# Kernel tuning notes

Hardware: AMD Instinct MI355X
Metric: run time of the kernel (lower is better)

Reference implementation:

```python
import jax, jax.numpy as jnp
import numpy as np

N_NODES = 100000
N_REL = 8
F_IN, F_HID, F_OUT = 64, 64, 32
N_EDGES = 1000000


def rgcn_conv(x, W, root, bias, src, dst, edge_type):
    """PyG RGCNConv with default aggr='mean': out[i] = sum_r mean_{j in N_r(i)} W_r x_j + root x_i + bias."""
    R, _, O = W.shape
    N = x.shape[0]
    # Transform every node under every relation: [R, N, O]
    h = jnp.einsum('nf,rfo->rno', x, W)
    # Gather per-edge messages: [E, O]
    msg = h[edge_type, src]
    # Per-(relation, dst) mean aggregation via combined segment ids
    seg = edge_type * N + dst
    sums = jax.ops.segment_sum(msg, seg, num_segments=R * N).reshape(R, N, O)
    cnt = jax.ops.segment_sum(jnp.ones((msg.shape[0],), msg.dtype), seg,
                              num_segments=R * N).reshape(R, N, 1)
    mean = sums / jnp.maximum(cnt, 1.0)  # empty neighborhoods -> 0
    return mean.sum(axis=0) + x @ root + bias


def setup_inputs() -> dict:
    key = jax.random.key(0)
    ks = jax.random.split(key, 9)
    s = lambda fan: 1.0 / np.sqrt(fan)
    x = jax.random.normal(ks[0], (N_NODES, F_IN), jnp.float32)
    edge_index = jax.random.randint(ks[1], (2, N_EDGES), 0, N_NODES, jnp.int64)
    edge_type = jax.random.randint(ks[2], (N_EDGES,), 0, N_REL, jnp.int64)
    W1 = jax.random.normal(ks[3], (N_REL, F_IN, F_HID), jnp.float32) * s(F_IN)
    root1 = jax.random.normal(ks[4], (F_IN, F_HID), jnp.float32) * s(F_IN)
    b1 = jnp.zeros((F_HID,), jnp.float32)
    W2 = jax.random.normal(ks[5], (N_REL, F_HID, F_OUT), jnp.float32) * s(F_HID)
    root2 = jax.random.normal(ks[6], (F_HID, F_OUT), jnp.float32) * s(F_HID)
    b2 = jnp.zeros((F_OUT,), jnp.float32)
    return {"x": x, "W1": W1, "root1": root1, "b1": b1,
            "W2": W2, "root2": root2, "b2": b2,
            "edge_index": edge_index, "edge_type": edge_type}


def reference(x, W1, root1, b1, W2, root2, b2, edge_index, edge_type):
    src, dst = edge_index[0], edge_index[1]
    # encode (dropout is identity in eval mode)
    h = jax.nn.relu(rgcn_conv(x, W1, root1, b1, src, dst, edge_type))
    z = rgcn_conv(h, W2, root2, b2, src, dst, edge_type)
    # decode: gather-dot-product link scores over the same edge list
    return (z[src] * z[dst]).sum(axis=1)
```

## Files before the change

kernel.cpp:

```cpp
#include <hip/hip_runtime.h>

#define F_IN 64
#define F_HID 64
#define F_OUT 32
#define NREL 8
#define SCAP 6144
#define RCAP 7680
#define MAXBUCK 200
#define PA_PE 16

typedef __attribute__((ext_vector_type(8))) short bfrag;
typedef __attribute__((ext_vector_type(4))) float ffrag;

__device__ inline unsigned short f2bf(float f) {
  unsigned u = __float_as_uint(f);
  unsigned r = (u + 0x7fffu + ((u >> 16) & 1u)) >> 16;
  return (unsigned short)r;
}
__device__ inline unsigned bf16pair(float lo, float hi) {
  return (unsigned)f2bf(lo) | ((unsigned)f2bf(hi) << 16);
}
__device__ inline float bflo(unsigned u) { return __uint_as_float(u << 16); }
__device__ inline float bfhi(unsigned u) { return __uint_as_float(u & 0xffff0000u); }

__device__ inline void acc8(float (&acc)[8], float s, uint4 g) {
  acc[0] += s * bflo(g.x); acc[1] += s * bfhi(g.x);
  acc[2] += s * bflo(g.y); acc[3] += s * bfhi(g.y);
  acc[4] += s * bflo(g.z); acc[5] += s * bfhi(g.z);
  acc[6] += s * bflo(g.w); acc[7] += s * bfhi(g.w);
}
__device__ inline float dot8(uint4 a, uint4 b) {
  return bflo(a.x) * bflo(b.x) + bfhi(a.x) * bfhi(b.x) +
         bflo(a.y) * bflo(b.y) + bfhi(a.y) * bfhi(b.y) +
         bflo(a.z) * bflo(b.z) + bfhi(a.z) * bfhi(b.z) +
         bflo(a.w) * bflo(b.w) + bfhi(a.w) * bfhi(b.w);
}

__global__ __launch_bounds__(256) void init_gcur(int* __restrict__ gcur, int nbuck) {
  int i = blockIdx.x * blockDim.x + threadIdx.x;
  if (i < nbuck) gcur[i] = i * SCAP;
}

__global__ __launch_bounds__(256) void binA_kernel(
    const int* __restrict__ src, const int* __restrict__ dst,
    const int* __restrict__ et, int* __restrict__ gcur,
    unsigned* __restrict__ staging, int E) {
  __shared__ int hist[MAXBUCK * 4];
  __shared__ int wbase[MAXBUCK * 4];
  const int tid = threadIdx.x;
  const int wave = tid >> 6;
  for (int i = tid; i < MAXBUCK * 4; i += 256) hist[i] = 0;
  __syncthreads();
  const int base = blockIdx.x * (256 * PA_PE);
  int dv[PA_PE], rk[PA_PE];
#pragma unroll
  for (int j = 0; j < PA_PE; ++j) {
    int e = base + j * 256 + tid;
    if (e < E) {
      int d = dst[e];
      dv[j] = d;
      rk[j] = atomicAdd(&hist[(d >> 9) * 4 + wave], 1);
    } else {
      dv[j] = -1;
    }
  }
  __syncthreads();
  for (int b = tid; b < MAXBUCK; b += 256) {
    int h0 = hist[b * 4 + 0], h1 = hist[b * 4 + 1];
    int h2 = hist[b * 4 + 2], h3 = hist[b * 4 + 3];
    int tot = h0 + h1 + h2 + h3;
    int gb = tot ? atomicAdd(&gcur[b], tot) : 0;
    wbase[b * 4 + 0] = gb;
    wbase[b * 4 + 1] = gb + h0;
    wbase[b * 4 + 2] = gb + h0 + h1;
    wbase[b * 4 + 3] = gb + h0 + h1 + h2;
  }
  __syncthreads();
#pragma unroll
  for (int j = 0; j < PA_PE; ++j) {
    if (dv[j] >= 0) {
      int e = base + j * 256 + tid;
      unsigned pk = (unsigned)src[e] | ((unsigned)et[e] << 17) |
                    ((unsigned)(dv[j] & 511) << 20);
      staging[wbase[(dv[j] >> 9) * 4 + wave] + rk[j]] = pk;
    }
  }
}

__global__ __launch_bounds__(256) void binB_kernel(
    const unsigned* __restrict__ staging, const int* __restrict__ gcur,
    int2* __restrict__ rec, int* __restrict__ startsA, int* __restrict__ endsA,
    int N) {
  __shared__ int cnt8[512 * 8];
  __shared__ int cur[512];
  __shared__ int tsum[256];
  const int b = blockIdx.x;
  const int tid = threadIdx.x;
  const int n0 = b << 9;
  const int nn = min(512, N - n0);
  const int cnt_b = gcur[b] - b * SCAP;
  const unsigned* st = staging + (size_t)b * SCAP;
  for (int i = tid; i < 512 * 8; i += 256) cnt8[i] = 0;
  __syncthreads();
  for (int i = tid; i < cnt_b; i += 256) {
    unsigned e = st[i];
    atomicAdd(&cnt8[((e >> 20) & 511) * 8 + ((e >> 17) & 7)], 1);
  }
  __syncthreads();
  const int na = 2 * tid, nb = 2 * tid + 1;
  int deg0 = 0, deg1 = 0;
#pragma unroll
  for (int r = 0; r < 8; ++r) {
    deg0 += cnt8[na * 8 + r];
    deg1 += cnt8[nb * 8 + r];
  }
  const int pd0 = (deg0 + 3) & ~3, pd1 = (deg1 + 3) & ~3;
  tsum[tid] = pd0 + pd1;
  __syncthreads();
  for (int off = 1; off < 256; off <<= 1) {
    int v = (tid >= off) ? tsum[tid - off] : 0;
    __syncthreads();
    tsum[tid] += v;
    __syncthreads();
  }
  const int excl = tsum[tid] - (pd0 + pd1);
  const int s0 = b * RCAP + excl;
  const int s1 = s0 + pd0;
  if (na < nn) { startsA[n0 + na] = s0; endsA[n0 + na] = s0 + pd0; cur[na] = s0; }
  if (nb < nn) { startsA[n0 + nb] = s1; endsA[n0 + nb] = s1 + pd1; cur[nb] = s1; }
  __syncthreads();
  for (int i = tid; i < 512 * 8; i += 256) {
    int cc = cnt8[i];
    ((float*)cnt8)[i] = cc > 0 ? 1.0f / (float)cc : 0.0f;
  }
  __syncthreads();
  for (int i = tid; i < cnt_b; i += 256) {
    unsigned e = st[i];
    int s = e & 0x1FFFF;
    int r = (e >> 17) & 7;
    int dl = (e >> 20) & 511;
    int pos = atomicAdd(&cur[dl], 1);
    rec[pos] = make_int2(r * N + s, ((const int*)cnt8)[dl * 8 + r]);
  }
  __syncthreads();
  if (na < nn) for (int p = cur[na]; p < s0 + pd0; ++p) rec[p] = make_int2(0, 0);
  if (nb < nn) for (int p = cur[nb]; p < s1 + pd1; ++p) rec[p] = make_int2(0, 0);
}

__global__ __launch_bounds__(256) void cvt_bf16_kernel(
    const float* __restrict__ in, unsigned* __restrict__ out, int n8) {
  int i = blockIdx.x * blockDim.x + threadIdx.x;
  if (i >= n8) return;
  const float4* p = (const float4*)(in + (size_t)i * 8);
  float4 a = p[0], b = p[1];
  uint4 o;
  o.x = bf16pair(a.x, a.y);
  o.y = bf16pair(a.z, a.w);
  o.z = bf16pair(b.x, b.y);
  o.w = bf16pair(b.z, b.w);
  *((uint4*)out + i) = o;
}

template <int O>
__global__ __launch_bounds__(256) void wprep_kernel(
    const float* __restrict__ W, unsigned short* __restrict__ Wf, int nrel) {
  constexpr int CT = O / 16;
  int t = blockIdx.x * blockDim.x + threadIdx.x;
  if (t >= nrel * CT * 2 * 64) return;
  int l = t & 63;
  int s = (t >> 6) & 1;
  int rc = t >> 7;
  int c = rc % CT;
  int r = rc / CT;
  const float* wsrc = W + (size_t)r * 64 * O;
  unsigned short* dst = Wf + (size_t)t * 8;
  int col = c * 16 + (l & 15);
  int k0 = s * 32 + ((l >> 4) * 8);
#pragma unroll
  for (int j = 0; j < 8; ++j) dst[j] = f2bf(wsrc[(size_t)(k0 + j) * O + col]);
}

template <int O>
__global__ __launch_bounds__(256) void mfma_transform_kernel(
    const unsigned short* __restrict__ Xb, const unsigned short* __restrict__ Wf,
    unsigned short* __restrict__ H, int N) {
  constexpr int CT = O / 16;
  constexpr int PAD = (O == 32) ? 40 : 72;
  __shared__ unsigned short tile[64 * PAD];
  const int w = threadIdx.x >> 6;
  const int l = threadIdx.x & 63;
  const int nb = blockIdx.x * 64;
  int arow = nb + w * 16 + (l & 15);
  if (arow >= N) arow = N - 1;
  const unsigned short* xp = Xb + (size_t)arow * 64 + ((l >> 4) * 8);
  bfrag a0 = *(const bfrag*)(xp);
  bfrag a1 = *(const bfrag*)(xp + 32);
  const int row = threadIdx.x >> 2, seg = threadIdx.x & 3;
  for (int r = 0; r < NREL + 1; ++r) {
    const unsigned short* wb = Wf + ((size_t)r * CT * 2 * 64 + l) * 8;
    ffrag acc[CT];
#pragma unroll
    for (int c = 0; c < CT; ++c) {
      bfrag b0 = *(const bfrag*)(wb + (size_t)(c * 2 + 0) * 512);
      bfrag b1 = *(const bfrag*)(wb + (size_t)(c * 2 + 1) * 512);
      ffrag z = {0.f, 0.f, 0.f, 0.f};
      acc[c] = __builtin_amdgcn_mfma_f32_16x16x32_bf16(a0, b0, z, 0, 0, 0);
      acc[c] = __builtin_amdgcn_mfma_f32_16x16x32_bf16(a1, b1, acc[c], 0, 0, 0);
    }
#pragma unroll
    for (int c = 0; c < CT; ++c)
#pragma unroll
      for (int i = 0; i < 4; ++i)
        tile[(w * 16 + (l >> 4) * 4 + i) * PAD + c * 16 + (l & 15)] = f2bf(acc[c][i]);
    __syncthreads();
    if (nb + row < N) {
      if (O == 64) {
        const uint4* sp = (const uint4*)(tile + row * PAD + seg * 16);
        uint4* gp = (uint4*)(H + ((size_t)r * N + nb + row) * 64 + seg * 16);
        gp[0] = sp[0];
        gp[1] = sp[1];
      } else {
        *(uint4*)(H + ((size_t)r * N + nb + row) * O + seg * 8) =
            *(const uint4*)(tile + row * PAD + seg * 8);
      }
    }
    __syncthreads();
  }
}

template <int O, bool RELU>
__global__ __launch_bounds__(256) void csr_agg_kernel(
    const unsigned* __restrict__ H, const int* __restrict__ startsA,
    const int* __restrict__ endsA, const int2* __restrict__ rec,
    const float* __restrict__ bias, unsigned* __restrict__ Y, int N) {
  constexpr int C = O / 8;
  constexpr int NPB = 256 / C;
  constexpr int HROW = O / 2;
  int t = threadIdx.x;
  int n = blockIdx.x * NPB + t / C;
  int c = t % C;
  if (n >= N) return;
  float acc[8];
  uint4 rr = *(const uint4*)(H + ((size_t)(NREL * N) + n) * HROW + c * 4);
  acc[0] = bias[c * 8 + 0] + bflo(rr.x);
  acc[1] = bias[c * 8 + 1] + bfhi(rr.x);
  acc[2] = bias[c * 8 + 2] + bflo(rr.y);
  acc[3] = bias[c * 8 + 3] + bfhi(rr.y);
  acc[4] = bias[c * 8 + 4] + bflo(rr.z);
  acc[5] = bias[c * 8 + 5] + bfhi(rr.z);
  acc[6] = bias[c * 8 + 6] + bflo(rr.w);
  acc[7] = bias[c * 8 + 7] + bfhi(rr.w);
  int p = startsA[n];
  int end = endsA[n];
  for (; p < end; p += 4) {
    int4 e01 = *(const int4*)(rec + p);
    int4 e23 = *(const int4*)(rec + p + 2);
    uint4 g0 = *(const uint4*)(H + (size_t)e01.x * HROW + c * 4);
    uint4 g1 = *(const uint4*)(H + (size_t)e01.z * HROW + c * 4);
    uint4 g2 = *(const uint4*)(H + (size_t)e23.x * HROW + c * 4);
    uint4 g3 = *(const uint4*)(H + (size_t)e23.z * HROW + c * 4);
    acc8(acc, __int_as_float(e01.y), g0);
    acc8(acc, __int_as_float(e01.w), g1);
    acc8(acc, __int_as_float(e23.y), g2);
    acc8(acc, __int_as_float(e23.w), g3);
  }
  if (RELU) {
#pragma unroll
    for (int j = 0; j < 8; ++j) acc[j] = fmaxf(acc[j], 0.f);
  }
  uint4 o;
  o.x = bf16pair(acc[0], acc[1]);
  o.y = bf16pair(acc[2], acc[3]);
  o.z = bf16pair(acc[4], acc[5]);
  o.w = bf16pair(acc[6], acc[7]);
  *(uint4*)(Y + (size_t)n * HROW + c * 4) = o;
}

__global__ __launch_bounds__(256) void decode_kernel(
    const unsigned* __restrict__ Z, const int* __restrict__ src,
    const int* __restrict__ dst, float* __restrict__ out, int E) {
  int e = blockIdx.x * blockDim.x + threadIdx.x;
  if (e >= E) return;
  const uint4* zs = (const uint4*)(Z + (size_t)src[e] * 16);
  const uint4* zd = (const uint4*)(Z + (size_t)dst[e] * 16);
  uint4 a0 = zs[0], a1 = zs[1], a2 = zs[2], a3 = zs[3];
  uint4 b0 = zd[0], b1 = zd[1], b2 = zd[2], b3 = zd[3];
  out[e] = dot8(a0, b0) + dot8(a1, b1) + dot8(a2, b2) + dot8(a3, b3);
}

extern "C" void kernel_launch(void* const* d_in, const int* in_sizes, int n_in,
                              void* d_out, int out_size, void* d_ws, size_t ws_size,
                              hipStream_t stream) {
  const float* x     = (const float*)d_in[0];
  const float* W1    = (const float*)d_in[1];
  const float* root1 = (const float*)d_in[2];
  const float* b1    = (const float*)d_in[3];
  const float* W2    = (const float*)d_in[4];
  const float* root2 = (const float*)d_in[5];
  const float* b2    = (const float*)d_in[6];
  const int*   ei    = (const int*)d_in[7];
  const int*   et    = (const int*)d_in[8];

  const int N = in_sizes[0] / F_IN;
  const int E = in_sizes[8];
  const int nbuck = (N + 511) >> 9;
  const int* srcp = ei;
  const int* dstp = ei + E;

  char* ws = (char*)d_ws;
  int*            gcur    = (int*)(ws + 0);
  unsigned*       staging = (unsigned*)(ws + 4096);
  int*            startsA = (int*)(ws + 4849664);
  int*            endsA   = (int*)(ws + 5249664);
  int2*           rec     = (int2*)(ws + 5649664);
  unsigned short* xb      = (unsigned short*)(ws + 17691904);
  unsigned short* wf1     = (unsigned short*)(ws + 30491904);
  unsigned short* wf2     = (unsigned short*)(ws + 30565632);
  unsigned short* h       = (unsigned short*)(ws + 30602496);
  unsigned short* hmid    = (unsigned short*)(ws + 145802496);
  unsigned short* z       = (unsigned short*)(ws + 158602496);

  init_gcur<<<1, 256, 0, stream>>>(gcur, nbuck);
  binA_kernel<<<(E + 256 * PA_PE - 1) / (256 * PA_PE), 256, 0, stream>>>(
      srcp, dstp, et, gcur, staging, E);
  binB_kernel<<<nbuck, 256, 0, stream>>>(staging, gcur, rec, startsA, endsA, N);

  cvt_bf16_kernel<<<(N * (F_IN / 8) + 255) / 256, 256, 0, stream>>>(
      x, (unsigned*)xb, N * (F_IN / 8));
  wprep_kernel<F_HID><<<16, 256, 0, stream>>>(W1, wf1, NREL);
  wprep_kernel<F_HID><<<2, 256, 0, stream>>>(root1, wf1 + (size_t)NREL * 4 * 2 * 64 * 8, 1);
  wprep_kernel<F_OUT><<<8, 256, 0, stream>>>(W2, wf2, NREL);
  wprep_kernel<F_OUT><<<1, 256, 0, stream>>>(root2, wf2 + (size_t)NREL * 2 * 2 * 64 * 8, 1);

  mfma_transform_kernel<F_HID>
      <<<(N + 63) / 64, 256, 0, stream>>>(xb, wf1, h, N);
  csr_agg_kernel<F_HID, true>
      <<<(N + 31) / 32, 256, 0, stream>>>((const unsigned*)h, startsA, endsA, rec,
                                          b1, (unsigned*)hmid, N);

  mfma_transform_kernel<F_OUT>
      <<<(N + 63) / 64, 256, 0, stream>>>(hmid, wf2, h, N);
  csr_agg_kernel<F_OUT, false>
      <<<(N + 63) / 64, 256, 0, stream>>>((const unsigned*)h, startsA, endsA, rec,
                                          b2, (unsigned*)z, N);

  decode_kernel<<<(E + 255) / 256, 256, 0, stream>>>((const unsigned*)z, srcp, dstp,
                                                     (float*)d_out, E);
}
```

Baseline: 182.7 us.

## Fuse prep kernels, fold bf16 conversion into transform, unroll CSR gather by eight

Merges weight preparation for both layers and the bucket-cursor initialization into a single prep kernel. The first transform now reads fp32 x directly and converts it to bf16 in registers, which removes the separate conversion kernel and its round trip through memory. The per-node record lists are padded to multiples of eight (with RCAP enlarged to fit) so the aggregation loop can issue eight gathers per iteration, adding memory-level parallelism. The cost is extra zero-padded records to read, and more registers per thread in the aggregation loop.

```diff
diff --git a/kernel.cpp b/kernel.cpp
--- a/kernel.cpp
+++ b/kernel.cpp
@@ -5,7 +5,7 @@
 #define F_OUT 32
 #define NREL 8
 #define SCAP 6144
-#define RCAP 7680
+#define RCAP 10240
 #define MAXBUCK 200
 #define PA_PE 16
 
@@ -36,9 +36,40 @@
          bflo(a.w) * bflo(b.w) + bfhi(a.w) * bfhi(b.w);
 }
 
-__global__ __launch_bounds__(256) void init_gcur(int* __restrict__ gcur, int nbuck) {
-  int i = blockIdx.x * blockDim.x + threadIdx.x;
-  if (i < nbuck) gcur[i] = i * SCAP;
+template <int O>
+__device__ inline void wprep_one(int t, const float* __restrict__ W,
+                                 const float* __restrict__ root,
+                                 unsigned short* __restrict__ Wf) {
+  constexpr int CT = O / 16;
+  int l = t & 63;
+  int s = (t >> 6) & 1;
+  int rc = t >> 7;
+  int c = rc % CT;
+  int r = rc / CT;
+  const float* wsrc = (r < NREL) ? W + (size_t)r * 64 * O : root;
+  unsigned short* dst = Wf + (size_t)t * 8;
+  int col = c * 16 + (l & 15);
+  int k0 = s * 32 + ((l >> 4) * 8);
+#pragma unroll
+  for (int j = 0; j < 8; ++j) dst[j] = f2bf(wsrc[(size_t)(k0 + j) * O + col]);
+}
+
+__global__ __launch_bounds__(256) void prep_kernel(
+    const float* __restrict__ W1, const float* __restrict__ root1,
+    const float* __restrict__ W2, const float* __restrict__ root2,
+    unsigned short* __restrict__ wf1, unsigned short* __restrict__ wf2,
+    int* __restrict__ gcur, int nbuck) {
+  int gid = blockIdx.x * 256 + threadIdx.x;
+  const int J1 = (NREL + 1) * (F_HID / 16) * 2 * 64;
+  const int J2 = (NREL + 1) * (F_OUT / 16) * 2 * 64;
+  if (gid < J1) {
+    wprep_one<F_HID>(gid, W1, root1, wf1);
+  } else if (gid < J1 + J2) {
+    wprep_one<F_OUT>(gid - J1, W2, root2, wf2);
+  } else if (gid - J1 - J2 < nbuck) {
+    int b = gid - J1 - J2;
+    gcur[b] = b * SCAP;
+  }
 }
 
 __global__ __launch_bounds__(256) void binA_kernel(
@@ -114,7 +145,7 @@
     deg0 += cnt8[na * 8 + r];
     deg1 += cnt8[nb * 8 + r];
   }
-  const int pd0 = (deg0 + 3) & ~3, pd1 = (deg1 + 3) & ~3;
+  const int pd0 = (deg0 + 7) & ~7, pd1 = (deg1 + 7) & ~7;
   tsum[tid] = pd0 + pd1;
   __syncthreads();
   for (int off = 1; off < 256; off <<= 1) {
@@ -147,42 +178,9 @@
   if (nb < nn) for (int p = cur[nb]; p < s1 + pd1; ++p) rec[p] = make_int2(0, 0);
 }
 
-__global__ __launch_bounds__(256) void cvt_bf16_kernel(
-    const float* __restrict__ in, unsigned* __restrict__ out, int n8) {
-  int i = blockIdx.x * blockDim.x + threadIdx.x;
-  if (i >= n8) return;
-  const float4* p = (const float4*)(in + (size_t)i * 8);
-  float4 a = p[0], b = p[1];
-  uint4 o;
-  o.x = bf16pair(a.x, a.y);
-  o.y = bf16pair(a.z, a.w);
-  o.z = bf16pair(b.x, b.y);
-  o.w = bf16pair(b.z, b.w);
-  *((uint4*)out + i) = o;
-}
-
-template <int O>
-__global__ __launch_bounds__(256) void wprep_kernel(
-    const float* __restrict__ W, unsigned short* __restrict__ Wf, int nrel) {
-  constexpr int CT = O / 16;
-  int t = blockIdx.x * blockDim.x + threadIdx.x;
-  if (t >= nrel * CT * 2 * 64) return;
-  int l = t & 63;
-  int s = (t >> 6) & 1;
-  int rc = t >> 7;
-  int c = rc % CT;
-  int r = rc / CT;
-  const float* wsrc = W + (size_t)r * 64 * O;
-  unsigned short* dst = Wf + (size_t)t * 8;
-  int col = c * 16 + (l & 15);
-  int k0 = s * 32 + ((l >> 4) * 8);
-#pragma unroll
-  for (int j = 0; j < 8; ++j) dst[j] = f2bf(wsrc[(size_t)(k0 + j) * O + col]);
-}
-
-template <int O>
+template <int O, bool F32IN>
 __global__ __launch_bounds__(256) void mfma_transform_kernel(
-    const unsigned short* __restrict__ Xb, const unsigned short* __restrict__ Wf,
+    const void* __restrict__ Xv, const unsigned short* __restrict__ Wf,
     unsigned short* __restrict__ H, int N) {
   constexpr int CT = O / 16;
   constexpr int PAD = (O == 32) ? 40 : 72;
@@ -192,9 +190,26 @@
   const int nb = blockIdx.x * 64;
   int arow = nb + w * 16 + (l & 15);
   if (arow >= N) arow = N - 1;
-  const unsigned short* xp = Xb + (size_t)arow * 64 + ((l >> 4) * 8);
-  bfrag a0 = *(const bfrag*)(xp);
-  bfrag a1 = *(const bfrag*)(xp + 32);
+  bfrag a0, a1;
+  if (F32IN) {
+    const float* xf = (const float*)Xv + (size_t)arow * 64 + ((l >> 4) * 8);
+    float4 v0 = *(const float4*)(xf);
+    float4 v1 = *(const float4*)(xf + 4);
+    float4 v2 = *(const float4*)(xf + 32);
+    float4 v3 = *(const float4*)(xf + 36);
+    a0[0] = (short)f2bf(v0.x); a0[1] = (short)f2bf(v0.y);
+    a0[2] = (short)f2bf(v0.z); a0[3] = (short)f2bf(v0.w);
+    a0[4] = (short)f2bf(v1.x); a0[5] = (short)f2bf(v1.y);
+    a0[6] = (short)f2bf(v1.z); a0[7] = (short)f2bf(v1.w);
+    a1[0] = (short)f2bf(v2.x); a1[1] = (short)f2bf(v2.y);
+    a1[2] = (short)f2bf(v2.z); a1[3] = (short)f2bf(v2.w);
+    a1[4] = (short)f2bf(v3.x); a1[5] = (short)f2bf(v3.y);
+    a1[6] = (short)f2bf(v3.z); a1[7] = (short)f2bf(v3.w);
+  } else {
+    const unsigned short* xp = (const unsigned short*)Xv + (size_t)arow * 64 + ((l >> 4) * 8);
+    a0 = *(const bfrag*)(xp);
+    a1 = *(const bfrag*)(xp + 32);
+  }
   const int row = threadIdx.x >> 2, seg = threadIdx.x & 3;
   for (int r = 0; r < NREL + 1; ++r) {
     const unsigned short* wb = Wf + ((size_t)r * CT * 2 * 64 + l) * 8;
@@ -252,17 +267,27 @@
   acc[7] = bias[c * 8 + 7] + bfhi(rr.w);
   int p = startsA[n];
   int end = endsA[n];
-  for (; p < end; p += 4) {
+  for (; p < end; p += 8) {
     int4 e01 = *(const int4*)(rec + p);
     int4 e23 = *(const int4*)(rec + p + 2);
+    int4 e45 = *(const int4*)(rec + p + 4);
+    int4 e67 = *(const int4*)(rec + p + 6);
     uint4 g0 = *(const uint4*)(H + (size_t)e01.x * HROW + c * 4);
     uint4 g1 = *(const uint4*)(H + (size_t)e01.z * HROW + c * 4);
     uint4 g2 = *(const uint4*)(H + (size_t)e23.x * HROW + c * 4);
     uint4 g3 = *(const uint4*)(H + (size_t)e23.z * HROW + c * 4);
+    uint4 g4 = *(const uint4*)(H + (size_t)e45.x * HROW + c * 4);
+    uint4 g5 = *(const uint4*)(H + (size_t)e45.z * HROW + c * 4);
+    uint4 g6 = *(const uint4*)(H + (size_t)e67.x * HROW + c * 4);
+    uint4 g7 = *(const uint4*)(H + (size_t)e67.z * HROW + c * 4);
     acc8(acc, __int_as_float(e01.y), g0);
     acc8(acc, __int_as_float(e01.w), g1);
     acc8(acc, __int_as_float(e23.y), g2);
     acc8(acc, __int_as_float(e23.w), g3);
+    acc8(acc, __int_as_float(e45.y), g4);
+    acc8(acc, __int_as_float(e45.w), g5);
+    acc8(acc, __int_as_float(e67.y), g6);
+    acc8(acc, __int_as_float(e67.w), g7);
   }
   if (RELU) {
 #pragma unroll
@@ -310,35 +335,27 @@
   char* ws = (char*)d_ws;
   int*            gcur    = (int*)(ws + 0);
   unsigned*       staging = (unsigned*)(ws + 4096);
-  int*            startsA = (int*)(ws + 4849664);
-  int*            endsA   = (int*)(ws + 5249664);
-  int2*           rec     = (int2*)(ws + 5649664);
-  unsigned short* xb      = (unsigned short*)(ws + 17691904);
-  unsigned short* wf1     = (unsigned short*)(ws + 30491904);
-  unsigned short* wf2     = (unsigned short*)(ws + 30565632);
-  unsigned short* h       = (unsigned short*)(ws + 30602496);
-  unsigned short* hmid    = (unsigned short*)(ws + 145802496);
-  unsigned short* z       = (unsigned short*)(ws + 158602496);
-
-  init_gcur<<<1, 256, 0, stream>>>(gcur, nbuck);
+  int*            startsA = (int*)(ws + 4919296);
+  int*            endsA   = (int*)(ws + 5319296);
+  int2*           rec     = (int2*)(ws + 5719296);
+  unsigned short* wf1     = (unsigned short*)(ws + 21775616);
+  unsigned short* wf2     = (unsigned short*)(ws + 21849344);
+  unsigned short* h       = (unsigned short*)(ws + 21886208);
+  unsigned short* hmid    = (unsigned short*)(ws + 137086208);
+  unsigned short* z       = (unsigned short*)(ws + 149886208);
+
+  prep_kernel<<<28, 256, 0, stream>>>(W1, root1, W2, root2, wf1, wf2, gcur, nbuck);
   binA_kernel<<<(E + 256 * PA_PE - 1) / (256 * PA_PE), 256, 0, stream>>>(
       srcp, dstp, et, gcur, staging, E);
   binB_kernel<<<nbuck, 256, 0, stream>>>(staging, gcur, rec, startsA, endsA, N);
 
-  cvt_bf16_kernel<<<(N * (F_IN / 8) + 255) / 256, 256, 0, stream>>>(
-      x, (unsigned*)xb, N * (F_IN / 8));
-  wprep_kernel<F_HID><<<16, 256, 0, stream>>>(W1, wf1, NREL);
-  wprep_kernel<F_HID><<<2, 256, 0, stream>>>(root1, wf1 + (size_t)NREL * 4 * 2 * 64 * 8, 1);
-  wprep_kernel<F_OUT><<<8, 256, 0, stream>>>(W2, wf2, NREL);
-  wprep_kernel<F_OUT><<<1, 256, 0, stream>>>(root2, wf2 + (size_t)NREL * 2 * 2 * 64 * 8, 1);
-
-  mfma_transform_kernel<F_HID>
-      <<<(N + 63) / 64, 256, 0, stream>>>(xb, wf1, h, N);
+  mfma_transform_kernel<F_HID, true>
+      <<<(N + 63) / 64, 256, 0, stream>>>(x, wf1, h, N);
   csr_agg_kernel<F_HID, true>
       <<<(N + 31) / 32, 256, 0, stream>>>((const unsigned*)h, startsA, endsA, rec,
                                           b1, (unsigned*)hmid, N);
 
-  mfma_transform_kernel<F_OUT>
+  mfma_transform_kernel<F_OUT, false>
       <<<(N + 63) / 64, 256, 0, stream>>>(hmid, wf2, h, N);
   csr_agg_kernel<F_OUT, false>
       <<<(N + 63) / 64, 256, 0, stream>>>((const unsigned*)h, startsA, endsA, rec,
```

Result: faster. 174.2 us (-4.6%).
